# Kernel optimization log

Hardware: AMD Instinct MI355X
Metric: run time of the kernel (lower is better)

## Reference

```python
import jax, jax.numpy as jnp
import numpy as np

TOP_K = 2


def setup_inputs() -> dict:
    key = jax.random.key(0)
    ks = jax.random.split(key, 6)
    B, S, H, I, E = 2, 1024, 1024, 2048, 8
    s_h = 1.0 / np.sqrt(H)
    s_i = 1.0 / np.sqrt(I)
    return {
        "x": jax.random.normal(ks[0], (B, S, H), jnp.float32),
        "gate_w": jax.random.normal(ks[1], (H, E), jnp.float32) * s_h,
        "gate_b": jnp.zeros((E,), jnp.float32),
        "w1": jax.random.normal(ks[2], (E, H, I), jnp.float32) * s_h,
        "w3": jax.random.normal(ks[3], (E, H, I), jnp.float32) * s_h,
        "w2": jax.random.normal(ks[4], (E, I, H), jnp.float32) * s_i,
    }


def reference(x, gate_w, gate_b, w1, w3, w2):
    # Gating: softmax over experts, then top-k selection + renormalization.
    logits = jnp.einsum("bsh,he->bse", x, gate_w) + gate_b            # [B,S,E]
    probs = jax.nn.softmax(logits, axis=-1)
    topk_w, topk_idx = jax.lax.top_k(probs, TOP_K)                    # [B,S,K]
    topk_w = topk_w / jnp.sum(topk_w, axis=-1, keepdims=True)

    E = gate_w.shape[-1]
    # Per-token combine weight for each expert (0 if not routed there).
    # one_hot: [B,S,K,E] -> combine: [B,S,E]
    combine = jnp.sum(jax.nn.one_hot(topk_idx, E, dtype=x.dtype) * topk_w[..., None], axis=-2)

    # SwiGLU expert FFN: down(silu(gate(x)) * up(x)); dense-masked reference
    # (compute every expert on every token, weight by combine; math identical
    # to the original gather/scatter loop since combine is 0 off-route).
    out = jnp.zeros_like(x)
    for e in range(E):
        h = jax.nn.silu(x @ w1[e]) * (x @ w3[e])                      # [B,S,I]
        out = out + combine[..., e:e + 1] * (h @ w2[e])               # [B,S,H]
    return out
```

## Files before the change

kernel.cpp:

```cpp
#include <hip/hip_runtime.h>
#include <hip/hip_bf16.h>
#include <math.h>

typedef __attribute__((ext_vector_type(4))) float f32x4;
typedef __attribute__((ext_vector_type(8))) short bf16x8;

#define T_TOK 2048
#define H_DIM 1024
#define I_DIM 2048
#define E_NUM 8

__device__ inline unsigned short f2bf(float f) {
  union { float f; unsigned int u; } v; v.f = f;
  unsigned int r = v.u + 0x7fffu + ((v.u >> 16) & 1u);
  return (unsigned short)(r >> 16);
}

__device__ inline void gld16(const void* g, void* l) {
  __builtin_amdgcn_global_load_lds((const __attribute__((address_space(1))) void*)g,
                                   (__attribute__((address_space(3))) void*)l, 16, 0, 0);
}

__global__ __launch_bounds__(256) void gate_kernel(
    const float* __restrict__ x, const float* __restrict__ gw, const float* __restrict__ gb,
    int* __restrict__ rec_e, float* __restrict__ rec_w)
{
  int wv = threadIdx.x >> 6, lane = threadIdx.x & 63;
  int t = blockIdx.x * 4 + wv;
  const float* xr = x + (size_t)t * H_DIM;
  float acc[8];
#pragma unroll
  for (int e = 0; e < 8; ++e) acc[e] = 0.f;
  for (int i = 0; i < H_DIM / 64; ++i) {
    int h = i * 64 + lane;
    float xv = xr[h];
    const float4* g = (const float4*)(gw + (size_t)h * 8);
    float4 g0 = g[0], g1 = g[1];
    acc[0] += xv * g0.x; acc[1] += xv * g0.y; acc[2] += xv * g0.z; acc[3] += xv * g0.w;
    acc[4] += xv * g1.x; acc[5] += xv * g1.y; acc[6] += xv * g1.z; acc[7] += xv * g1.w;
  }
#pragma unroll
  for (int s = 1; s < 64; s <<= 1) {
#pragma unroll
    for (int e = 0; e < 8; ++e) acc[e] += __shfl_xor(acc[e], s);
  }
  if (lane == 0) {
    float l[8];
#pragma unroll
    for (int e = 0; e < 8; ++e) l[e] = acc[e] + gb[e];
    int e0 = 0;
    for (int e = 1; e < 8; ++e) if (l[e] > l[e0]) e0 = e;
    int e1 = (e0 == 0) ? 1 : 0;
    for (int e = 0; e < 8; ++e) if (e != e0 && l[e] > l[e1]) e1 = e;
    float w0 = 1.f / (1.f + expf(l[e1] - l[e0]));
    rec_e[t * 2]     = e0; rec_e[t * 2 + 1] = e1;
    rec_w[t * 2]     = w0; rec_w[t * 2 + 1] = 1.f - w0;
  }
}

__global__ __launch_bounds__(256) void route_kernel(
    const int* __restrict__ rec_e, const float* __restrict__ rec_w,
    int* __restrict__ counts_g, int* __restrict__ list_tok, float* __restrict__ list_w)
{
  __shared__ int cnt[8], base[8], fill[8];
  int tid = threadIdx.x;
  if (tid < 8) { cnt[tid] = 0; fill[tid] = 0; }
  __syncthreads();
  for (int i = tid; i < T_TOK * 2; i += 256) atomicAdd(&cnt[rec_e[i]], 1);
  __syncthreads();
  if (tid == 0) {
    int b = 0;
    for (int e = 0; e < 8; ++e) { base[e] = b; b += cnt[e]; }
  }
  if (tid < 8) counts_g[tid] = cnt[tid];
  __syncthreads();
  for (int i = tid; i < T_TOK * 2; i += 256) {
    int e = rec_e[i];
    int pos = atomicAdd(&fill[e], 1);
    list_tok[base[e] + pos] = i;
    list_w[base[e] + pos]   = rec_w[i];
  }
}

__global__ __launch_bounds__(256) void cast_x(const float* __restrict__ in,
                                              unsigned short* __restrict__ outp)
{
  int i = (blockIdx.x * 256 + threadIdx.x) * 4;
  float4 v = *(const float4*)(in + i);
  ushort4 o;
  o.x = f2bf(v.x); o.y = f2bf(v.y); o.z = f2bf(v.z); o.w = f2bf(v.w);
  *(ushort4*)(outp + i) = o;
}

__global__ __launch_bounds__(256) void transpose13(
    const float* __restrict__ w1, const float* __restrict__ w3,
    unsigned short* __restrict__ w1t, unsigned short* __restrict__ w3t)
{
  __shared__ float tile[32][33];
  int z = blockIdx.z;
  const float* ip = (z < 8 ? w1 : w3) + (size_t)(z & 7) * H_DIM * I_DIM;
  unsigned short* op = (z < 8 ? w1t : w3t) + (size_t)(z & 7) * H_DIM * I_DIM;
  const int R = H_DIM, C = I_DIM;
  int c0 = blockIdx.x * 32, r0 = blockIdx.y * 32;
  int tx = threadIdx.x & 31, ty = threadIdx.x >> 5;
#pragma unroll
  for (int j = 0; j < 4; ++j)
    tile[ty + 8 * j][tx] = ip[(size_t)(r0 + ty + 8 * j) * C + c0 + tx];
  __syncthreads();
#pragma unroll
  for (int j = 0; j < 4; ++j)
    op[(size_t)(c0 + ty + 8 * j) * R + r0 + tx] = f2bf(tile[tx][ty + 8 * j]);
}

__global__ __launch_bounds__(256) void transpose2(
    const float* __restrict__ w2, unsigned short* __restrict__ w2t)
{
  __shared__ float tile[32][33];
  int e = blockIdx.z;
  const float* ip = w2 + (size_t)e * I_DIM * H_DIM;
  unsigned short* op = w2t + (size_t)e * I_DIM * H_DIM;
  const int R = I_DIM, C = H_DIM;
  int c0 = blockIdx.x * 32, r0 = blockIdx.y * 32;
  int tx = threadIdx.x & 31, ty = threadIdx.x >> 5;
#pragma unroll
  for (int j = 0; j < 4; ++j)
    tile[ty + 8 * j][tx] = ip[(size_t)(r0 + ty + 8 * j) * C + c0 + tx];
  __syncthreads();
#pragma unroll
  for (int j = 0; j < 4; ++j)
    op[(size_t)(c0 + ty + 8 * j) * R + r0 + tx] = f2bf(tile[tx][ty + 8 * j]);
}

__global__ __launch_bounds__(256) void gemm1(
    const unsigned short* __restrict__ xb,
    const unsigned short* __restrict__ w1t,
    const unsigned short* __restrict__ w3t,
    const int* __restrict__ counts,
    const int* __restrict__ list_tok,
    unsigned short* __restrict__ hbuf)
{
  int e = blockIdx.z;
  int nbase = 0;
#pragma unroll
  for (int i = 0; i < 8; ++i) if (i < e) nbase += counts[i];
  int n_e = counts[e];
  int t0 = blockIdx.y * 128;
  if (t0 >= n_e) return;
  int i0 = blockIdx.x * 64;

  __shared__ __align__(16) unsigned short As[128 * 32];
  __shared__ __align__(16) unsigned short B1s[64 * 32];
  __shared__ __align__(16) unsigned short B3s[64 * 32];

  int tid = threadIdx.x;
  int r = tid >> 2;
  int seg = (tid & 3) * 8;

  int sr0 = t0 + r;       if (sr0 >= n_e) sr0 = n_e - 1;
  int sr1 = t0 + 64 + r;  if (sr1 >= n_e) sr1 = n_e - 1;
  int tok0 = list_tok[nbase + sr0] >> 1;
  int tok1 = list_tok[nbase + sr1] >> 1;
  const char* gA0 = (const char*)(xb + (size_t)tok0 * H_DIM + seg);
  const char* gA1 = (const char*)(xb + (size_t)tok1 * H_DIM + seg);
  const char* gB1 = (const char*)(w1t + ((size_t)e * I_DIM + i0 + r) * H_DIM + seg);
  const char* gB3 = (const char*)(w3t + ((size_t)e * I_DIM + i0 + r) * H_DIM + seg);

  char* lA0 = (char*)As + tid * 16;
  char* lA1 = (char*)As + 4096 + tid * 16;
  char* lB1 = (char*)B1s + tid * 16;
  char* lB3 = (char*)B3s + tid * 16;

  int w = tid >> 6, lane = tid & 63, lm = lane & 15, lq = lane >> 4;
  int wm = w & 1, wn = w >> 1;

  f32x4 acc1[4][2], acc3[4][2];
#pragma unroll
  for (int i = 0; i < 4; ++i)
#pragma unroll
    for (int j = 0; j < 2; ++j) { acc1[i][j] = (f32x4){0,0,0,0}; acc3[i][j] = (f32x4){0,0,0,0}; }

  for (int kb = 0; kb < H_DIM; kb += 32) {
    __syncthreads();
    gld16(gA0 + kb * 2, lA0);
    gld16(gA1 + kb * 2, lA1);
    gld16(gB1 + kb * 2, lB1);
    gld16(gB3 + kb * 2, lB3);
    __syncthreads();
    bf16x8 a[4], b1[2], b3[2];
#pragma unroll
    for (int i = 0; i < 4; ++i)
      a[i] = *(const bf16x8*)((const char*)As + 2 * ((wm * 64 + i * 16 + lm) * 32 + lq * 8));
#pragma unroll
    for (int j = 0; j < 2; ++j) {
      b1[j] = *(const bf16x8*)((const char*)B1s + 2 * ((wn * 32 + j * 16 + lm) * 32 + lq * 8));
      b3[j] = *(const bf16x8*)((const char*)B3s + 2 * ((wn * 32 + j * 16 + lm) * 32 + lq * 8));
    }
#pragma unroll
    for (int i = 0; i < 4; ++i)
#pragma unroll
      for (int j = 0; j < 2; ++j) {
        acc1[i][j] = __builtin_amdgcn_mfma_f32_16x16x32_bf16(a[i], b1[j], acc1[i][j], 0, 0, 0);
        acc3[i][j] = __builtin_amdgcn_mfma_f32_16x16x32_bf16(a[i], b3[j], acc3[i][j], 0, 0, 0);
      }
  }

#pragma unroll
  for (int i = 0; i < 4; ++i) {
#pragma unroll
    for (int rr = 0; rr < 4; ++rr) {
      int slot = t0 + wm * 64 + i * 16 + lq * 4 + rr;
      if (slot < n_e) {
#pragma unroll
        for (int j = 0; j < 2; ++j) {
          float g = acc1[i][j][rr], u = acc3[i][j][rr];
          float hv = (g / (1.f + __expf(-g))) * u;
          hbuf[(size_t)(nbase + slot) * I_DIM + i0 + wn * 32 + j * 16 + lm] = f2bf(hv);
        }
      }
    }
  }
}

__global__ __launch_bounds__(256) void gemm2(
    const unsigned short* __restrict__ hbuf,
    const unsigned short* __restrict__ w2t,
    const int* __restrict__ counts,
    const int* __restrict__ list_tok,
    const float* __restrict__ list_w,
    float* __restrict__ partial)
{
  int e = blockIdx.z;
  int nbase = 0;
#pragma unroll
  for (int i = 0; i < 8; ++i) if (i < e) nbase += counts[i];
  int n_e = counts[e];
  int t0 = blockIdx.y * 64;
  if (t0 >= n_e) return;
  int h0 = blockIdx.x * 128;

  __shared__ __align__(16) unsigned short As[64 * 32];
  __shared__ __align__(16) unsigned short Bs[128 * 32];

  int tid = threadIdx.x;
  int r = tid >> 2;
  int seg = (tid & 3) * 8;

  int sr = t0 + r; if (sr >= n_e) sr = n_e - 1;
  const char* gA  = (const char*)(hbuf + (size_t)(nbase + sr) * I_DIM + seg);
  const char* gB0 = (const char*)(w2t + ((size_t)e * H_DIM + h0 + r) * I_DIM + seg);
  const char* gB1 = (const char*)(w2t + ((size_t)e * H_DIM + h0 + 64 + r) * I_DIM + seg);

  char* lA  = (char*)As + tid * 16;
  char* lB0 = (char*)Bs + tid * 16;
  char* lB1 = (char*)Bs + 4096 + tid * 16;

  int w = tid >> 6, lane = tid & 63, lm = lane & 15, lq = lane >> 4;
  int wm = w & 1, wn = (w >> 1) * 64;

  f32x4 acc[2][4];
#pragma unroll
  for (int i = 0; i < 2; ++i)
#pragma unroll
    for (int j = 0; j < 4; ++j) acc[i][j] = (f32x4){0,0,0,0};

  for (int kb = 0; kb < I_DIM; kb += 32) {
    __syncthreads();
    gld16(gA + kb * 2, lA);
    gld16(gB0 + kb * 2, lB0);
    gld16(gB1 + kb * 2, lB1);
    __syncthreads();
    bf16x8 a[2], b[4];
#pragma unroll
    for (int i = 0; i < 2; ++i)
      a[i] = *(const bf16x8*)((const char*)As + 2 * ((wm * 32 + i * 16 + lm) * 32 + lq * 8));
#pragma unroll
    for (int j = 0; j < 4; ++j)
      b[j] = *(const bf16x8*)((const char*)Bs + 2 * ((wn + j * 16 + lm) * 32 + lq * 8));
#pragma unroll
    for (int i = 0; i < 2; ++i)
#pragma unroll
      for (int j = 0; j < 4; ++j)
        acc[i][j] = __builtin_amdgcn_mfma_f32_16x16x32_bf16(a[i], b[j], acc[i][j], 0, 0, 0);
  }

  int entv[2][4]; float wtv[2][4];
#pragma unroll
  for (int i = 0; i < 2; ++i)
#pragma unroll
    for (int rr = 0; rr < 4; ++rr) {
      int slot = t0 + wm * 32 + i * 16 + lq * 4 + rr;
      if (slot < n_e) { entv[i][rr] = list_tok[nbase + slot]; wtv[i][rr] = list_w[nbase + slot]; }
      else entv[i][rr] = -1;
    }
#pragma unroll
  for (int i = 0; i < 2; ++i)
#pragma unroll
    for (int j = 0; j < 4; ++j)
#pragma unroll
      for (int rr = 0; rr < 4; ++rr) {
        if (entv[i][rr] >= 0) {
          int t = entv[i][rr] >> 1, kk = entv[i][rr] & 1;
          partial[((size_t)kk * T_TOK + t) * H_DIM + h0 + wn + j * 16 + lm] = acc[i][j][rr] * wtv[i][rr];
        }
      }
}

__global__ __launch_bounds__(256) void combine(const float* __restrict__ partial,
                                               float* __restrict__ out)
{
  int i = (blockIdx.x * 256 + threadIdx.x) * 4;
  float4 a = *(const float4*)(partial + i);
  float4 b = *(const float4*)(partial + (size_t)T_TOK * H_DIM + i);
  float4 o;
  o.x = a.x + b.x; o.y = a.y + b.y; o.z = a.z + b.z; o.w = a.w + b.w;
  *(float4*)(out + i) = o;
}

extern "C" void kernel_launch(void* const* d_in, const int* in_sizes, int n_in,
                              void* d_out, int out_size, void* d_ws, size_t ws_size,
                              hipStream_t stream) {
  const float* x  = (const float*)d_in[0];
  const float* gw = (const float*)d_in[1];
  const float* gb = (const float*)d_in[2];
  const float* w1 = (const float*)d_in[3];
  const float* w3 = (const float*)d_in[4];
  const float* w2 = (const float*)d_in[5];
  float* out = (float*)d_out;

  char* ws = (char*)d_ws;
  int*   counts   = (int*)(ws);
  int*   rec_e    = (int*)(ws + 128);
  float* rec_w    = (float*)(ws + 16512);
  int*   list_tok = (int*)(ws + 32896);
  float* list_w   = (float*)(ws + 49280);
  const size_t MB = 1024ull * 1024ull;
  unsigned short* xb   = (unsigned short*)(ws + 1 * MB);
  unsigned short* w1t  = (unsigned short*)(ws + 5 * MB);
  unsigned short* w3t  = (unsigned short*)(ws + 37 * MB);
  unsigned short* w2t  = (unsigned short*)(ws + 69 * MB);
  unsigned short* hbuf = (unsigned short*)(ws + 101 * MB);
  float* partial       = (float*)(ws + 117 * MB);

  gate_kernel<<<T_TOK / 4, 256, 0, stream>>>(x, gw, gb, rec_e, rec_w);
  route_kernel<<<1, 256, 0, stream>>>(rec_e, rec_w, counts, list_tok, list_w);
  cast_x<<<(T_TOK * H_DIM) / (256 * 4), 256, 0, stream>>>(x, xb);
  transpose13<<<dim3(I_DIM / 32, H_DIM / 32, 16), 256, 0, stream>>>(w1, w3, w1t, w3t);
  transpose2<<<dim3(H_DIM / 32, I_DIM / 32, 8), 256, 0, stream>>>(w2, w2t);
  gemm1<<<dim3(I_DIM / 64, 16, E_NUM), 256, 0, stream>>>(xb, w1t, w3t, counts, list_tok, hbuf);
  gemm2<<<dim3(H_DIM / 128, 32, E_NUM), 256, 0, stream>>>(hbuf, w2t, counts, list_tok, list_w, partial);
  combine<<<(T_TOK * H_DIM) / (256 * 4), 256, 0, stream>>>(partial, out);
}
```

Baseline: 380.8 us.

## Fuse x cast into gating, merge transposes, split-K gemm2, widen grids

Folds the bf16 cast of x into the gating kernel and merges the two weight transposes into one launch with float4 loads and paired bf16 stores. The route kernel now counts per thread in registers before a single shared atomic per expert. gemm2 is split over K into two halves that write four partial planes, which combine4 sums, and the gemm1 and gemm2 grids gain more y blocks for occupancy. The partial buffer is placed over w1t's memory, which gemm1 no longer needs by then. The aim is fewer launches, better transpose memory efficiency and more parallelism, at the cost of extra partial-buffer traffic.

```diff
diff --git a/kernel.cpp b/kernel.cpp
--- a/kernel.cpp
+++ b/kernel.cpp
@@ -23,17 +23,19 @@
 
 __global__ __launch_bounds__(256) void gate_kernel(
     const float* __restrict__ x, const float* __restrict__ gw, const float* __restrict__ gb,
-    int* __restrict__ rec_e, float* __restrict__ rec_w)
+    int* __restrict__ rec_e, float* __restrict__ rec_w, unsigned short* __restrict__ xb)
 {
   int wv = threadIdx.x >> 6, lane = threadIdx.x & 63;
   int t = blockIdx.x * 4 + wv;
   const float* xr = x + (size_t)t * H_DIM;
+  unsigned short* xo = xb + (size_t)t * H_DIM;
   float acc[8];
 #pragma unroll
   for (int e = 0; e < 8; ++e) acc[e] = 0.f;
   for (int i = 0; i < H_DIM / 64; ++i) {
     int h = i * 64 + lane;
     float xv = xr[h];
+    xo[h] = f2bf(xv);
     const float4* g = (const float4*)(gw + (size_t)h * 8);
     float4 g0 = g[0], g1 = g[1];
     acc[0] += xv * g0.x; acc[1] += xv * g0.y; acc[2] += xv * g0.z; acc[3] += xv * g0.w;
@@ -66,7 +68,17 @@
   int tid = threadIdx.x;
   if (tid < 8) { cnt[tid] = 0; fill[tid] = 0; }
   __syncthreads();
-  for (int i = tid; i < T_TOK * 2; i += 256) atomicAdd(&cnt[rec_e[i]], 1);
+  int e_loc[16];
+  int c_loc[8];
+#pragma unroll
+  for (int e = 0; e < 8; ++e) c_loc[e] = 0;
+#pragma unroll
+  for (int it = 0; it < 16; ++it) {
+    e_loc[it] = rec_e[it * 256 + tid];
+    c_loc[e_loc[it] & 7]++;
+  }
+#pragma unroll
+  for (int e = 0; e < 8; ++e) if (c_loc[e]) atomicAdd(&cnt[e], c_loc[e]);
   __syncthreads();
   if (tid == 0) {
     int b = 0;
@@ -74,61 +86,50 @@
   }
   if (tid < 8) counts_g[tid] = cnt[tid];
   __syncthreads();
-  for (int i = tid; i < T_TOK * 2; i += 256) {
-    int e = rec_e[i];
+#pragma unroll
+  for (int it = 0; it < 16; ++it) {
+    int i = it * 256 + tid;
+    int e = e_loc[it] & 7;
     int pos = atomicAdd(&fill[e], 1);
     list_tok[base[e] + pos] = i;
     list_w[base[e] + pos]   = rec_w[i];
   }
 }
 
-__global__ __launch_bounds__(256) void cast_x(const float* __restrict__ in,
-                                              unsigned short* __restrict__ outp)
-{
-  int i = (blockIdx.x * 256 + threadIdx.x) * 4;
-  float4 v = *(const float4*)(in + i);
-  ushort4 o;
-  o.x = f2bf(v.x); o.y = f2bf(v.y); o.z = f2bf(v.z); o.w = f2bf(v.w);
-  *(ushort4*)(outp + i) = o;
-}
-
-__global__ __launch_bounds__(256) void transpose13(
-    const float* __restrict__ w1, const float* __restrict__ w3,
-    unsigned short* __restrict__ w1t, unsigned short* __restrict__ w3t)
+__global__ __launch_bounds__(256) void transpose_all(
+    const float* __restrict__ w1, const float* __restrict__ w3, const float* __restrict__ w2,
+    unsigned short* __restrict__ w1t, unsigned short* __restrict__ w3t,
+    unsigned short* __restrict__ w2t)
 {
   __shared__ float tile[32][33];
   int z = blockIdx.z;
-  const float* ip = (z < 8 ? w1 : w3) + (size_t)(z & 7) * H_DIM * I_DIM;
-  unsigned short* op = (z < 8 ? w1t : w3t) + (size_t)(z & 7) * H_DIM * I_DIM;
-  const int R = H_DIM, C = I_DIM;
-  int c0 = blockIdx.x * 32, r0 = blockIdx.y * 32;
-  int tx = threadIdx.x & 31, ty = threadIdx.x >> 5;
-#pragma unroll
-  for (int j = 0; j < 4; ++j)
-    tile[ty + 8 * j][tx] = ip[(size_t)(r0 + ty + 8 * j) * C + c0 + tx];
+  const float* ip; unsigned short* op; int R, C, c0, r0;
+  if (z < 16) {
+    ip = (z < 8 ? w1 : w3) + (size_t)(z & 7) * (H_DIM * I_DIM);
+    op = (z < 8 ? w1t : w3t) + (size_t)(z & 7) * (H_DIM * I_DIM);
+    R = H_DIM; C = I_DIM;
+    c0 = blockIdx.x * 32; r0 = blockIdx.y * 32;
+  } else {
+    ip = w2 + (size_t)(z - 16) * (H_DIM * I_DIM);
+    op = w2t + (size_t)(z - 16) * (H_DIM * I_DIM);
+    R = I_DIM; C = H_DIM;
+    int t2 = blockIdx.x + 64 * blockIdx.y;
+    c0 = (t2 & 31) * 32; r0 = (t2 >> 5) * 32;
+  }
+  int t = threadIdx.x;
+  int r = t >> 3, cq = (t & 7) * 4;
+  float4 v = *(const float4*)(ip + (size_t)(r0 + r) * C + c0 + cq);
+  tile[r][cq] = v.x; tile[r][cq + 1] = v.y; tile[r][cq + 2] = v.z; tile[r][cq + 3] = v.w;
   __syncthreads();
-#pragma unroll
-  for (int j = 0; j < 4; ++j)
-    op[(size_t)(c0 + ty + 8 * j) * R + r0 + tx] = f2bf(tile[tx][ty + 8 * j]);
-}
-
-__global__ __launch_bounds__(256) void transpose2(
-    const float* __restrict__ w2, unsigned short* __restrict__ w2t)
-{
-  __shared__ float tile[32][33];
-  int e = blockIdx.z;
-  const float* ip = w2 + (size_t)e * I_DIM * H_DIM;
-  unsigned short* op = w2t + (size_t)e * I_DIM * H_DIM;
-  const int R = I_DIM, C = H_DIM;
-  int c0 = blockIdx.x * 32, r0 = blockIdx.y * 32;
-  int tx = threadIdx.x & 31, ty = threadIdx.x >> 5;
-#pragma unroll
-  for (int j = 0; j < 4; ++j)
-    tile[ty + 8 * j][tx] = ip[(size_t)(r0 + ty + 8 * j) * C + c0 + tx];
-  __syncthreads();
-#pragma unroll
-  for (int j = 0; j < 4; ++j)
-    op[(size_t)(c0 + ty + 8 * j) * R + r0 + tx] = f2bf(tile[tx][ty + 8 * j]);
+  int rp = (t & 15) * 2, cc = t >> 4;
+#pragma unroll
+  for (int j = 0; j < 2; ++j) {
+    int c = cc + 16 * j;
+    ushort2 o;
+    o.x = f2bf(tile[rp][c]);
+    o.y = f2bf(tile[rp + 1][c]);
+    *(ushort2*)(op + (size_t)(c0 + c) * R + r0 + rp) = o;
+  }
 }
 
 __global__ __launch_bounds__(256) void gemm1(
@@ -234,9 +235,11 @@
 #pragma unroll
   for (int i = 0; i < 8; ++i) if (i < e) nbase += counts[i];
   int n_e = counts[e];
-  int t0 = blockIdx.y * 64;
+  int ts = blockIdx.y >> 1, kh = blockIdx.y & 1;
+  int t0 = ts * 64;
   if (t0 >= n_e) return;
   int h0 = blockIdx.x * 128;
+  int k0 = kh * (I_DIM / 2);
 
   __shared__ __align__(16) unsigned short As[64 * 32];
   __shared__ __align__(16) unsigned short Bs[128 * 32];
@@ -246,9 +249,9 @@
   int seg = (tid & 3) * 8;
 
   int sr = t0 + r; if (sr >= n_e) sr = n_e - 1;
-  const char* gA  = (const char*)(hbuf + (size_t)(nbase + sr) * I_DIM + seg);
-  const char* gB0 = (const char*)(w2t + ((size_t)e * H_DIM + h0 + r) * I_DIM + seg);
-  const char* gB1 = (const char*)(w2t + ((size_t)e * H_DIM + h0 + 64 + r) * I_DIM + seg);
+  const char* gA  = (const char*)(hbuf + (size_t)(nbase + sr) * I_DIM + k0 + seg);
+  const char* gB0 = (const char*)(w2t + ((size_t)e * H_DIM + h0 + r) * I_DIM + k0 + seg);
+  const char* gB1 = (const char*)(w2t + ((size_t)e * H_DIM + h0 + 64 + r) * I_DIM + k0 + seg);
 
   char* lA  = (char*)As + tid * 16;
   char* lB0 = (char*)Bs + tid * 16;
@@ -263,7 +266,7 @@
 #pragma unroll
     for (int j = 0; j < 4; ++j) acc[i][j] = (f32x4){0,0,0,0};
 
-  for (int kb = 0; kb < I_DIM; kb += 32) {
+  for (int kb = 0; kb < I_DIM / 2; kb += 32) {
     __syncthreads();
     gld16(gA + kb * 2, lA);
     gld16(gB0 + kb * 2, lB0);
@@ -300,19 +303,27 @@
       for (int rr = 0; rr < 4; ++rr) {
         if (entv[i][rr] >= 0) {
           int t = entv[i][rr] >> 1, kk = entv[i][rr] & 1;
-          partial[((size_t)kk * T_TOK + t) * H_DIM + h0 + wn + j * 16 + lm] = acc[i][j][rr] * wtv[i][rr];
+          int plane = kh * 2 + kk;
+          partial[((size_t)plane * T_TOK + t) * H_DIM + h0 + wn + j * 16 + lm] =
+              acc[i][j][rr] * wtv[i][rr];
         }
       }
 }
 
-__global__ __launch_bounds__(256) void combine(const float* __restrict__ partial,
-                                               float* __restrict__ out)
-{
+__global__ __launch_bounds__(256) void combine4(const float* __restrict__ partial,
+                                                float* __restrict__ out)
+{
+  const size_t P = (size_t)T_TOK * H_DIM;
   int i = (blockIdx.x * 256 + threadIdx.x) * 4;
   float4 a = *(const float4*)(partial + i);
-  float4 b = *(const float4*)(partial + (size_t)T_TOK * H_DIM + i);
+  float4 b = *(const float4*)(partial + P + i);
+  float4 c = *(const float4*)(partial + 2 * P + i);
+  float4 d = *(const float4*)(partial + 3 * P + i);
   float4 o;
-  o.x = a.x + b.x; o.y = a.y + b.y; o.z = a.z + b.z; o.w = a.w + b.w;
+  o.x = a.x + b.x + c.x + d.x;
+  o.y = a.y + b.y + c.y + d.y;
+  o.z = a.z + b.z + c.z + d.z;
+  o.w = a.w + b.w + c.w + d.w;
   *(float4*)(out + i) = o;
 }
 
@@ -336,17 +347,15 @@
   const size_t MB = 1024ull * 1024ull;
   unsigned short* xb   = (unsigned short*)(ws + 1 * MB);
   unsigned short* w1t  = (unsigned short*)(ws + 5 * MB);
+  float* partial       = (float*)(ws + 5 * MB);
   unsigned short* w3t  = (unsigned short*)(ws + 37 * MB);
   unsigned short* w2t  = (unsigned short*)(ws + 69 * MB);
   unsigned short* hbuf = (unsigned short*)(ws + 101 * MB);
-  float* partial       = (float*)(ws + 117 * MB);
-
-  gate_kernel<<<T_TOK / 4, 256, 0, stream>>>(x, gw, gb, rec_e, rec_w);
+
+  gate_kernel<<<T_TOK / 4, 256, 0, stream>>>(x, gw, gb, rec_e, rec_w, xb);
   route_kernel<<<1, 256, 0, stream>>>(rec_e, rec_w, counts, list_tok, list_w);
-  cast_x<<<(T_TOK * H_DIM) / (256 * 4), 256, 0, stream>>>(x, xb);
-  transpose13<<<dim3(I_DIM / 32, H_DIM / 32, 16), 256, 0, stream>>>(w1, w3, w1t, w3t);
-  transpose2<<<dim3(H_DIM / 32, I_DIM / 32, 8), 256, 0, stream>>>(w2, w2t);
-  gemm1<<<dim3(I_DIM / 64, 16, E_NUM), 256, 0, stream>>>(xb, w1t, w3t, counts, list_tok, hbuf);
-  gemm2<<<dim3(H_DIM / 128, 32, E_NUM), 256, 0, stream>>>(hbuf, w2t, counts, list_tok, list_w, partial);
-  combine<<<(T_TOK * H_DIM) / (256 * 4), 256, 0, stream>>>(partial, out);
-}
+  transpose_all<<<dim3(64, 32, 24), 256, 0, stream>>>(w1, w3, w2, w1t, w3t, w2t);
+  gemm1<<<dim3(I_DIM / 64, 32, E_NUM), 256, 0, stream>>>(xb, w1t, w3t, counts, list_tok, hbuf);
+  gemm2<<<dim3(H_DIM / 128, 128, E_NUM), 256, 0, stream>>>(hbuf, w2t, counts, list_tok, list_w, partial);
+  combine4<<<(T_TOK * H_DIM) / (256 * 4), 256, 0, stream>>>(partial, out);
+}
```

Measured after the change: 367.7 us. 1.04x faster.
